# Kernel tuning notes

Hardware: AMD Instinct MI355X
Metric: run time of the kernel (lower is better)

The kernel has to match this reference:

```python
import jax, jax.numpy as jnp
import numpy as np

NUM_GROUP = 512
GROUP_SIZE = 32


def setup_inputs() -> dict:
    key = jax.random.key(0)
    xyz = jax.random.normal(key, (16, 16384, 3), dtype=jnp.float32)
    return {"xyz": xyz}


def reference(xyz):
    B, N, _ = xyz.shape
    # misc.arange-style deterministic center sampling: evenly strided indices
    sel = jnp.arange(NUM_GROUP) * (N // NUM_GROUP)          # [G]
    center = xyz[:, sel, :]                                  # [B, G, 3]

    # squared pairwise distance: ||c||^2 + ||x||^2 - 2 c.x  -> [B, G, N]
    sqr = (-2.0 * jnp.einsum("bgc,bnc->bgn", center, xyz)
           + jnp.sum(center ** 2, axis=-1)[:, :, None]
           + jnp.sum(xyz ** 2, axis=-1)[:, None, :])

    # kNN: smallest K distances -> top_k on negated distances
    _, idx = jax.lax.top_k(-sqr, GROUP_SIZE)                 # [B, G, K]

    # gather neighborhoods per batch: xyz[b, idx[b,g,k], :]
    neighborhood = jax.vmap(lambda pts, i: pts[i])(xyz, idx)  # [B, G, K, 3]
    neighborhood = neighborhood - center[:, :, None, :]

    ids = jnp.broadcast_to(sel[None, :], (B, NUM_GROUP))     # [B, G]
    return neighborhood, center, ids
```

## Files before the change

### kernel.cpp

```cpp
#include <hip/hip_runtime.h>
#include <stdint.h>


#define TB     512
#define GB     8
#define PPT    32
#define NWAVE  (TB / 64)
#define CAP    224

typedef __attribute__((ext_vector_type(2))) float f32x2;

__global__ __launch_bounds__(TB) void group_knn_kernel(
    const float* __restrict__ xyz,
    float* __restrict__ out_nb,
    float* __restrict__ out_ctr,
    float* __restrict__ out_ids)
{
    const int NPTS = 16384;
    const int GSZ  = 32;

    const int blk = blockIdx.x;
    const int b   = blk >> 6;
    const int g0  = (blk & 63) * GB;
    const int t   = threadIdx.x;
    const int lane = t & 63;
    const int w    = t >> 6;

    const float* base = xyz + (size_t)b * NPTS * 3;

    f32x2 C0[GB / 2], C1[GB / 2], C2[GB / 2];
#pragma unroll
    for (int p = 0; p < GB / 2; ++p) {
        const int ncA = (g0 + 2 * p) * 32;
        const int ncB = (g0 + 2 * p + 1) * 32;
        C0[p] = (f32x2){ -2.0f * base[ncA * 3 + 0], -2.0f * base[ncB * 3 + 0] };
        C1[p] = (f32x2){ -2.0f * base[ncA * 3 + 1], -2.0f * base[ncB * 3 + 1] };
        C2[p] = (f32x2){ -2.0f * base[ncA * 3 + 2], -2.0f * base[ncB * 3 + 2] };
    }

    __shared__ unsigned long long s_cand[GB][CAP];
    __shared__ float s_t[GB][NWAVE];
    __shared__ int s_cnt[GB];
    __shared__ unsigned s_win[GB][GSZ];

    f32x2 m2[GB / 2];
#pragma unroll
    for (int p = 0; p < GB / 2; ++p)
        m2[p] = (f32x2){ __builtin_inff(), __builtin_inff() };

    for (int i = 0; i < PPT; i += 4) {
        float px[4][3];
#pragma unroll
        for (int u = 0; u < 4; ++u) {
            const int n = (i + u) * TB + t;
            const float* p = base + (size_t)n * 3;
            px[u][0] = p[0]; px[u][1] = p[1]; px[u][2] = p[2];
        }
#pragma unroll
        for (int u = 0; u < 4; ++u) {
            const float x0 = px[u][0], x1 = px[u][1], x2 = px[u][2];
            const float xs = __builtin_fmaf(x2, x2, __builtin_fmaf(x1, x1, x0 * x0));
            const f32x2 X0 = (f32x2){ x0, x0 };
            const f32x2 X1 = (f32x2){ x1, x1 };
            const f32x2 X2 = (f32x2){ x2, x2 };
            const f32x2 XS = (f32x2){ xs, xs };
#pragma unroll
            for (int p = 0; p < GB / 2; ++p) {
                const f32x2 s = C0[p] * X0 + (C1[p] * X1 + (C2[p] * X2 + XS));
                m2[p] = __builtin_elementwise_min(m2[p], s);
            }
        }
    }

#pragma unroll
    for (int q = 0; q < GB; ++q) {
        float v = (q & 1) ? m2[q >> 1].y : m2[q >> 1].x;
#pragma unroll
        for (int k = 2; k <= 64; k <<= 1) {
#pragma unroll
            for (int j = k >> 1; j > 0; j >>= 1) {
                const float o = __shfl_xor(v, j, 64);
                const bool up = ((lane & k) == 0);
                const bool takeMin = (((lane & j) == 0) == up);
                const float mn = fminf(v, o);
                const float mx = fmaxf(v, o);
                v = takeMin ? mn : mx;
            }
        }
        if (lane == 3) s_t[q][w] = v;
    }
    if (t < GB) s_cnt[t] = 0;
    __syncthreads();

    f32x2 T2[GB / 2];
#pragma unroll
    for (int p = 0; p < GB / 2; ++p) {
        float Ta = s_t[2 * p][0], Tb = s_t[2 * p + 1][0];
#pragma unroll
        for (int ww = 1; ww < NWAVE; ++ww) {
            Ta = fmaxf(Ta, s_t[2 * p][ww]);
            Tb = fmaxf(Tb, s_t[2 * p + 1][ww]);
        }
        T2[p] = (f32x2){ Ta, Tb };
    }

    for (int i = 0; i < PPT; i += 4) {
        float px[4][3];
#pragma unroll
        for (int u = 0; u < 4; ++u) {
            const int n = (i + u) * TB + t;
            const float* p = base + (size_t)n * 3;
            px[u][0] = p[0]; px[u][1] = p[1]; px[u][2] = p[2];
        }
#pragma unroll
        for (int u = 0; u < 4; ++u) {
            const int n = (i + u) * TB + t;
            const float x0 = px[u][0], x1 = px[u][1], x2 = px[u][2];
            const float xs = __builtin_fmaf(x2, x2, __builtin_fmaf(x1, x1, x0 * x0));
            const f32x2 X0 = (f32x2){ x0, x0 };
            const f32x2 X1 = (f32x2){ x1, x1 };
            const f32x2 X2 = (f32x2){ x2, x2 };
            const f32x2 XS = (f32x2){ xs, xs };
#pragma unroll
            for (int p = 0; p < GB / 2; ++p) {
                const f32x2 s = C0[p] * X0 + (C1[p] * X1 + (C2[p] * X2 + XS));
                if (s.x <= T2[p].x) {
                    unsigned uu = __float_as_uint(s.x);
                    uu ^= (unsigned)(((int)uu) >> 31) | 0x80000000u;
                    const int pos = atomicAdd(&s_cnt[2 * p], 1);
                    if (pos < CAP)
                        s_cand[2 * p][pos] = ((unsigned long long)uu << 32) | (unsigned)n;
                }
                if (s.y <= T2[p].y) {
                    unsigned uu = __float_as_uint(s.y);
                    uu ^= (unsigned)(((int)uu) >> 31) | 0x80000000u;
                    const int pos = atomicAdd(&s_cnt[2 * p + 1], 1);
                    if (pos < CAP)
                        s_cand[2 * p + 1][pos] = ((unsigned long long)uu << 32) | (unsigned)n;
                }
            }
        }
    }
    __syncthreads();

    {
        const int q = w;
        const int cnt = s_cnt[q];
        const float Tq = (q & 1) ? T2[q >> 1].y : T2[q >> 1].x;
        const float a0 = (q & 1) ? C0[q >> 1].y : C0[q >> 1].x;
        const float a1 = (q & 1) ? C1[q >> 1].y : C1[q >> 1].x;
        const float a2 = (q & 1) ? C2[q >> 1].y : C2[q >> 1].x;
        (void)Tq;
        if (cnt <= CAP) {
            for (int j = lane; j < cnt; j += 64) {
                const unsigned long long c = s_cand[q][j];
                int r = 0;
                for (int i = 0; i < cnt; ++i) r += (s_cand[q][i] < c) ? 1 : 0;
                if (r < GSZ) s_win[q][r] = (unsigned)c & 0xFFFFu;
            }
        } else {
            unsigned long long last = 0ull;
            for (int k = 0; k < GSZ; ++k) {
                unsigned long long best = ~0ull;
                for (int n = lane; n < NPTS; n += 64) {
                    const float x0 = base[n * 3 + 0];
                    const float x1 = base[n * 3 + 1];
                    const float x2 = base[n * 3 + 2];
                    const float xs = __builtin_fmaf(x2, x2,
                                     __builtin_fmaf(x1, x1, x0 * x0));
                    const float s = __builtin_fmaf(a0, x0,
                                    __builtin_fmaf(a1, x1,
                                    __builtin_fmaf(a2, x2, xs)));
                    unsigned uu = __float_as_uint(s);
                    uu ^= (unsigned)(((int)uu) >> 31) | 0x80000000u;
                    const unsigned long long kk =
                        ((unsigned long long)uu << 32) | (unsigned)n;
                    if (kk > last && kk < best) best = kk;
                }
#pragma unroll
                for (int mm = 32; mm >= 1; mm >>= 1) {
                    const unsigned long long o = __shfl_xor(best, mm, 64);
                    best = (o < best) ? o : best;
                }
                last = best;
                if (lane == 0) s_win[q][k] = (unsigned)best & 0xFFFFu;
            }
        }
    }
    __syncthreads();

    const int gbase = b * 512 + g0;
    if (t < GB * GSZ) {
        const int q  = t >> 5;
        const int tt = t & 31;
        const int nc = (g0 + q) * 32;
        const float cc0 = base[nc * 3 + 0];
        const float cc1 = base[nc * 3 + 1];
        const float cc2 = base[nc * 3 + 2];
        const unsigned n = s_win[q][tt];
        const float x0 = base[n * 3 + 0];
        const float x1 = base[n * 3 + 1];
        const float x2 = base[n * 3 + 2];
        const size_t ob = (((size_t)(gbase + q)) * GSZ + tt) * 3;
        out_nb[ob + 0] = x0 - cc0;
        out_nb[ob + 1] = x1 - cc1;
        out_nb[ob + 2] = x2 - cc2;
    } else if (t < GB * GSZ + GB * 3) {
        const int u = t - GB * GSZ;
        const int q = u / 3, c = u % 3;
        out_ctr[(size_t)(gbase + q) * 3 + c] = base[((g0 + q) * 32) * 3 + c];
    } else if (t < GB * GSZ + GB * 3 + GB) {
        const int q = t - (GB * GSZ + GB * 3);
        out_ids[gbase + q] = (float)((g0 + q) * 32);
    }
}

extern "C" void kernel_launch(void* const* d_in, const int* in_sizes, int n_in,
                              void* d_out, int out_size, void* d_ws, size_t ws_size,
                              hipStream_t stream) {
    const float* xyz = (const float*)d_in[0];
    float* out = (float*)d_out;
    float* out_nb  = out;
    float* out_ctr = out + 786432;
    float* out_ids = out + 786432 + 24576;
    hipLaunchKernelGGL(group_knn_kernel, dim3(16 * 512 / GB), dim3(TB), 0, stream,
                       xyz, out_nb, out_ctr, out_ids);
}
```

Measured before the change: 73.04 us.

## Halve block size and groups per block, add double-buffered point loads

Blocks shrink from 512 to 256 threads and handle 4 centers instead of 8, so 2048 blocks are launched and each thread scans 64 points. Both distance passes now use ping-pong register buffers so the next four points load while the current four are computed, aiming to hide global load latency. The per-wave threshold now takes the 8th-smallest value of each wave's 64 lanes instead of the 4th, so fewer candidates pass the filter with 4 waves. This also doubles the total point-scan work across blocks, since each center pair now rereads the whole cloud in more blocks. The fallback selection gets a small correctness fix for the first iteration.

After: 68.75 us. -5.9%, faster.

```diff
diff --git a/kernel.cpp b/kernel.cpp
--- a/kernel.cpp
+++ b/kernel.cpp
@@ -2,13 +2,77 @@
 #include <stdint.h>
 
 
-#define TB     512
-#define GB     8
-#define PPT    32
+#define TB     256
+#define GB     4
+#define PPT    64
 #define NWAVE  (TB / 64)
 #define CAP    224
 
 typedef __attribute__((ext_vector_type(2))) float f32x2;
+
+#define LOADP(dst, i)                                                    \
+    {                                                                    \
+        _Pragma("unroll")                                                \
+        for (int u = 0; u < 4; ++u) {                                    \
+            const int n = ((i) + u) * TB + t;                            \
+            const float* p = base + (size_t)n * 3;                       \
+            dst[u][0] = p[0]; dst[u][1] = p[1]; dst[u][2] = p[2];        \
+        }                                                                \
+    }
+
+#define COMPA(src)                                                       \
+    {                                                                    \
+        _Pragma("unroll")                                                \
+        for (int u = 0; u < 4; ++u) {                                    \
+            const float x0 = src[u][0], x1 = src[u][1], x2 = src[u][2];  \
+            const float xs = __builtin_fmaf(x2, x2,                      \
+                             __builtin_fmaf(x1, x1, x0 * x0));           \
+            const f32x2 X0 = (f32x2){ x0, x0 };                          \
+            const f32x2 X1 = (f32x2){ x1, x1 };                          \
+            const f32x2 X2 = (f32x2){ x2, x2 };                          \
+            const f32x2 XS = (f32x2){ xs, xs };                          \
+            _Pragma("unroll")                                            \
+            for (int p = 0; p < 2; ++p) {                                \
+                const f32x2 s = C0[p] * X0 + (C1[p] * X1 + (C2[p] * X2 + XS)); \
+                m2[p] = __builtin_elementwise_min(m2[p], s);             \
+            }                                                            \
+        }                                                                \
+    }
+
+#define COMPB(src, i)                                                    \
+    {                                                                    \
+        _Pragma("unroll")                                                \
+        for (int u = 0; u < 4; ++u) {                                    \
+            const int n = ((i) + u) * TB + t;                            \
+            const float x0 = src[u][0], x1 = src[u][1], x2 = src[u][2];  \
+            const float xs = __builtin_fmaf(x2, x2,                      \
+                             __builtin_fmaf(x1, x1, x0 * x0));           \
+            const f32x2 X0 = (f32x2){ x0, x0 };                          \
+            const f32x2 X1 = (f32x2){ x1, x1 };                          \
+            const f32x2 X2 = (f32x2){ x2, x2 };                          \
+            const f32x2 XS = (f32x2){ xs, xs };                          \
+            _Pragma("unroll")                                            \
+            for (int p = 0; p < 2; ++p) {                                \
+                const f32x2 s = C0[p] * X0 + (C1[p] * X1 + (C2[p] * X2 + XS)); \
+                if (s.x <= T2[p].x) {                                    \
+                    unsigned uu = __float_as_uint(s.x);                  \
+                    uu ^= (unsigned)(((int)uu) >> 31) | 0x80000000u;     \
+                    const int pos = atomicAdd(&s_cnt[2 * p], 1);         \
+                    if (pos < CAP)                                       \
+                        s_cand[2 * p][pos] =                             \
+                            ((unsigned long long)uu << 32) | (unsigned)n;\
+                }                                                        \
+                if (s.y <= T2[p].y) {                                    \
+                    unsigned uu = __float_as_uint(s.y);                  \
+                    uu ^= (unsigned)(((int)uu) >> 31) | 0x80000000u;     \
+                    const int pos = atomicAdd(&s_cnt[2 * p + 1], 1);     \
+                    if (pos < CAP)                                       \
+                        s_cand[2 * p + 1][pos] =                         \
+                            ((unsigned long long)uu << 32) | (unsigned)n;\
+                }                                                        \
+            }                                                            \
+        }                                                                \
+    }
 
 __global__ __launch_bounds__(TB) void group_knn_kernel(
     const float* __restrict__ xyz,
@@ -20,17 +84,17 @@
     const int GSZ  = 32;
 
     const int blk = blockIdx.x;
-    const int b   = blk >> 6;
-    const int g0  = (blk & 63) * GB;
+    const int b   = blk >> 7;
+    const int g0  = (blk & 127) * GB;
     const int t   = threadIdx.x;
     const int lane = t & 63;
     const int w    = t >> 6;
 
     const float* base = xyz + (size_t)b * NPTS * 3;
 
-    f32x2 C0[GB / 2], C1[GB / 2], C2[GB / 2];
-#pragma unroll
-    for (int p = 0; p < GB / 2; ++p) {
+    f32x2 C0[2], C1[2], C2[2];
+#pragma unroll
+    for (int p = 0; p < 2; ++p) {
         const int ncA = (g0 + 2 * p) * 32;
         const int ncB = (g0 + 2 * p + 1) * 32;
         C0[p] = (f32x2){ -2.0f * base[ncA * 3 + 0], -2.0f * base[ncB * 3 + 0] };
@@ -43,32 +107,19 @@
     __shared__ int s_cnt[GB];
     __shared__ unsigned s_win[GB][GSZ];
 
-    f32x2 m2[GB / 2];
-#pragma unroll
-    for (int p = 0; p < GB / 2; ++p)
+    f32x2 m2[2];
+#pragma unroll
+    for (int p = 0; p < 2; ++p)
         m2[p] = (f32x2){ __builtin_inff(), __builtin_inff() };
 
-    for (int i = 0; i < PPT; i += 4) {
-        float px[4][3];
-#pragma unroll
-        for (int u = 0; u < 4; ++u) {
-            const int n = (i + u) * TB + t;
-            const float* p = base + (size_t)n * 3;
-            px[u][0] = p[0]; px[u][1] = p[1]; px[u][2] = p[2];
-        }
-#pragma unroll
-        for (int u = 0; u < 4; ++u) {
-            const float x0 = px[u][0], x1 = px[u][1], x2 = px[u][2];
-            const float xs = __builtin_fmaf(x2, x2, __builtin_fmaf(x1, x1, x0 * x0));
-            const f32x2 X0 = (f32x2){ x0, x0 };
-            const f32x2 X1 = (f32x2){ x1, x1 };
-            const f32x2 X2 = (f32x2){ x2, x2 };
-            const f32x2 XS = (f32x2){ xs, xs };
-#pragma unroll
-            for (int p = 0; p < GB / 2; ++p) {
-                const f32x2 s = C0[p] * X0 + (C1[p] * X1 + (C2[p] * X2 + XS));
-                m2[p] = __builtin_elementwise_min(m2[p], s);
-            }
+    {
+        float pa[4][3], pb[4][3];
+        LOADP(pa, 0);
+        for (int i = 0; i < PPT; i += 8) {
+            LOADP(pb, i + 4);
+            COMPA(pa);
+            if (i + 8 < PPT) LOADP(pa, i + 8);
+            COMPA(pb);
         }
     }
 
@@ -87,14 +138,14 @@
                 v = takeMin ? mn : mx;
             }
         }
-        if (lane == 3) s_t[q][w] = v;
+        if (lane == 7) s_t[q][w] = v;
     }
     if (t < GB) s_cnt[t] = 0;
     __syncthreads();
 
-    f32x2 T2[GB / 2];
-#pragma unroll
-    for (int p = 0; p < GB / 2; ++p) {
+    f32x2 T2[2];
+#pragma unroll
+    for (int p = 0; p < 2; ++p) {
         float Ta = s_t[2 * p][0], Tb = s_t[2 * p + 1][0];
 #pragma unroll
         for (int ww = 1; ww < NWAVE; ++ww) {
@@ -104,41 +155,14 @@
         T2[p] = (f32x2){ Ta, Tb };
     }
 
-    for (int i = 0; i < PPT; i += 4) {
-        float px[4][3];
-#pragma unroll
-        for (int u = 0; u < 4; ++u) {
-            const int n = (i + u) * TB + t;
-            const float* p = base + (size_t)n * 3;
-            px[u][0] = p[0]; px[u][1] = p[1]; px[u][2] = p[2];
-        }
-#pragma unroll
-        for (int u = 0; u < 4; ++u) {
-            const int n = (i + u) * TB + t;
-            const float x0 = px[u][0], x1 = px[u][1], x2 = px[u][2];
-            const float xs = __builtin_fmaf(x2, x2, __builtin_fmaf(x1, x1, x0 * x0));
-            const f32x2 X0 = (f32x2){ x0, x0 };
-            const f32x2 X1 = (f32x2){ x1, x1 };
-            const f32x2 X2 = (f32x2){ x2, x2 };
-            const f32x2 XS = (f32x2){ xs, xs };
-#pragma unroll
-            for (int p = 0; p < GB / 2; ++p) {
-                const f32x2 s = C0[p] * X0 + (C1[p] * X1 + (C2[p] * X2 + XS));
-                if (s.x <= T2[p].x) {
-                    unsigned uu = __float_as_uint(s.x);
-                    uu ^= (unsigned)(((int)uu) >> 31) | 0x80000000u;
-                    const int pos = atomicAdd(&s_cnt[2 * p], 1);
-                    if (pos < CAP)
-                        s_cand[2 * p][pos] = ((unsigned long long)uu << 32) | (unsigned)n;
-                }
-                if (s.y <= T2[p].y) {
-                    unsigned uu = __float_as_uint(s.y);
-                    uu ^= (unsigned)(((int)uu) >> 31) | 0x80000000u;
-                    const int pos = atomicAdd(&s_cnt[2 * p + 1], 1);
-                    if (pos < CAP)
-                        s_cand[2 * p + 1][pos] = ((unsigned long long)uu << 32) | (unsigned)n;
-                }
-            }
+    {
+        float pa[4][3], pb[4][3];
+        LOADP(pa, 0);
+        for (int i = 0; i < PPT; i += 8) {
+            LOADP(pb, i + 4);
+            COMPB(pa, i);
+            if (i + 8 < PPT) LOADP(pa, i + 8);
+            COMPB(pb, i + 4);
         }
     }
     __syncthreads();
@@ -146,11 +170,9 @@
     {
         const int q = w;
         const int cnt = s_cnt[q];
-        const float Tq = (q & 1) ? T2[q >> 1].y : T2[q >> 1].x;
         const float a0 = (q & 1) ? C0[q >> 1].y : C0[q >> 1].x;
         const float a1 = (q & 1) ? C1[q >> 1].y : C1[q >> 1].x;
         const float a2 = (q & 1) ? C2[q >> 1].y : C2[q >> 1].x;
-        (void)Tq;
         if (cnt <= CAP) {
             for (int j = lane; j < cnt; j += 64) {
                 const unsigned long long c = s_cand[q][j];
@@ -175,7 +197,7 @@
                     uu ^= (unsigned)(((int)uu) >> 31) | 0x80000000u;
                     const unsigned long long kk =
                         ((unsigned long long)uu << 32) | (unsigned)n;
-                    if (kk > last && kk < best) best = kk;
+                    if ((k == 0 || kk > last) && kk < best) best = kk;
                 }
 #pragma unroll
                 for (int mm = 32; mm >= 1; mm >>= 1) {
@@ -223,6 +245,6 @@
     float* out_nb  = out;
     float* out_ctr = out + 786432;
     float* out_ids = out + 786432 + 24576;
-    hipLaunchKernelGGL(group_knn_kernel, dim3(16 * 512 / GB), dim3(TB), 0, stream,
+    hipLaunchKernelGGL(group_knn_kernel, dim3(2048), dim3(TB), 0, stream,
                        xyz, out_nb, out_ctr, out_ids);
 }
```

## Shrink blocks to two groups and 128 threads with more points per thread

Applied to the files above, without the earlier changes.

Each block now handles 2 centers with 128 threads instead of 8 centers with 512 threads, and each thread scans 128 points. The launch grows to 4096 blocks. The threshold now uses the 16th-smallest per-wave minimum, and the candidate capacity rises to 320. The aim is more blocks and lower per-block register and shared-memory pressure. The cost is that every point load is shared by only 2 centers instead of 8, so global/L2 traffic per unit of distance work roughly quadruples. The looser threshold also yields more candidates for the quadratic rank step. It also fixes the fallback selection so the first pick accepts key zero.

Result: slower. 77.07 us (+5.5%).

```diff
diff --git a/kernel.cpp b/kernel.cpp
--- a/kernel.cpp
+++ b/kernel.cpp
@@ -2,11 +2,11 @@
 #include <stdint.h>
 
 
-#define TB     512
-#define GB     8
-#define PPT    32
+#define TB     128
+#define GB     2
+#define PPT    128
 #define NWAVE  (TB / 64)
-#define CAP    224
+#define CAP    320
 
 typedef __attribute__((ext_vector_type(2))) float f32x2;
 
@@ -20,22 +20,21 @@
     const int GSZ  = 32;
 
     const int blk = blockIdx.x;
-    const int b   = blk >> 6;
-    const int g0  = (blk & 63) * GB;
+    const int b   = blk >> 8;
+    const int g0  = (blk & 255) * GB;
     const int t   = threadIdx.x;
     const int lane = t & 63;
     const int w    = t >> 6;
 
     const float* base = xyz + (size_t)b * NPTS * 3;
 
-    f32x2 C0[GB / 2], C1[GB / 2], C2[GB / 2];
-#pragma unroll
-    for (int p = 0; p < GB / 2; ++p) {
-        const int ncA = (g0 + 2 * p) * 32;
-        const int ncB = (g0 + 2 * p + 1) * 32;
-        C0[p] = (f32x2){ -2.0f * base[ncA * 3 + 0], -2.0f * base[ncB * 3 + 0] };
-        C1[p] = (f32x2){ -2.0f * base[ncA * 3 + 1], -2.0f * base[ncB * 3 + 1] };
-        C2[p] = (f32x2){ -2.0f * base[ncA * 3 + 2], -2.0f * base[ncB * 3 + 2] };
+    f32x2 C0, C1, C2;
+    {
+        const int ncA = g0 * 32;
+        const int ncB = (g0 + 1) * 32;
+        C0 = (f32x2){ -2.0f * base[ncA * 3 + 0], -2.0f * base[ncB * 3 + 0] };
+        C1 = (f32x2){ -2.0f * base[ncA * 3 + 1], -2.0f * base[ncB * 3 + 1] };
+        C2 = (f32x2){ -2.0f * base[ncA * 3 + 2], -2.0f * base[ncB * 3 + 2] };
     }
 
     __shared__ unsigned long long s_cand[GB][CAP];
@@ -43,10 +42,7 @@
     __shared__ int s_cnt[GB];
     __shared__ unsigned s_win[GB][GSZ];
 
-    f32x2 m2[GB / 2];
-#pragma unroll
-    for (int p = 0; p < GB / 2; ++p)
-        m2[p] = (f32x2){ __builtin_inff(), __builtin_inff() };
+    f32x2 m2 = (f32x2){ __builtin_inff(), __builtin_inff() };
 
     for (int i = 0; i < PPT; i += 4) {
         float px[4][3];
@@ -64,17 +60,14 @@
             const f32x2 X1 = (f32x2){ x1, x1 };
             const f32x2 X2 = (f32x2){ x2, x2 };
             const f32x2 XS = (f32x2){ xs, xs };
-#pragma unroll
-            for (int p = 0; p < GB / 2; ++p) {
-                const f32x2 s = C0[p] * X0 + (C1[p] * X1 + (C2[p] * X2 + XS));
-                m2[p] = __builtin_elementwise_min(m2[p], s);
-            }
+            const f32x2 s = C0 * X0 + (C1 * X1 + (C2 * X2 + XS));
+            m2 = __builtin_elementwise_min(m2, s);
         }
     }
 
 #pragma unroll
     for (int q = 0; q < GB; ++q) {
-        float v = (q & 1) ? m2[q >> 1].y : m2[q >> 1].x;
+        float v = (q & 1) ? m2.y : m2.x;
 #pragma unroll
         for (int k = 2; k <= 64; k <<= 1) {
 #pragma unroll
@@ -87,21 +80,20 @@
                 v = takeMin ? mn : mx;
             }
         }
-        if (lane == 3) s_t[q][w] = v;
+        if (lane == 15) s_t[q][w] = v;
     }
     if (t < GB) s_cnt[t] = 0;
     __syncthreads();
 
-    f32x2 T2[GB / 2];
-#pragma unroll
-    for (int p = 0; p < GB / 2; ++p) {
-        float Ta = s_t[2 * p][0], Tb = s_t[2 * p + 1][0];
+    f32x2 T2;
+    {
+        float Ta = s_t[0][0], Tb = s_t[1][0];
 #pragma unroll
         for (int ww = 1; ww < NWAVE; ++ww) {
-            Ta = fmaxf(Ta, s_t[2 * p][ww]);
-            Tb = fmaxf(Tb, s_t[2 * p + 1][ww]);
-        }
-        T2[p] = (f32x2){ Ta, Tb };
+            Ta = fmaxf(Ta, s_t[0][ww]);
+            Tb = fmaxf(Tb, s_t[1][ww]);
+        }
+        T2 = (f32x2){ Ta, Tb };
     }
 
     for (int i = 0; i < PPT; i += 4) {
@@ -121,23 +113,20 @@
             const f32x2 X1 = (f32x2){ x1, x1 };
             const f32x2 X2 = (f32x2){ x2, x2 };
             const f32x2 XS = (f32x2){ xs, xs };
-#pragma unroll
-            for (int p = 0; p < GB / 2; ++p) {
-                const f32x2 s = C0[p] * X0 + (C1[p] * X1 + (C2[p] * X2 + XS));
-                if (s.x <= T2[p].x) {
-                    unsigned uu = __float_as_uint(s.x);
-                    uu ^= (unsigned)(((int)uu) >> 31) | 0x80000000u;
-                    const int pos = atomicAdd(&s_cnt[2 * p], 1);
-                    if (pos < CAP)
-                        s_cand[2 * p][pos] = ((unsigned long long)uu << 32) | (unsigned)n;
-                }
-                if (s.y <= T2[p].y) {
-                    unsigned uu = __float_as_uint(s.y);
-                    uu ^= (unsigned)(((int)uu) >> 31) | 0x80000000u;
-                    const int pos = atomicAdd(&s_cnt[2 * p + 1], 1);
-                    if (pos < CAP)
-                        s_cand[2 * p + 1][pos] = ((unsigned long long)uu << 32) | (unsigned)n;
-                }
+            const f32x2 s = C0 * X0 + (C1 * X1 + (C2 * X2 + XS));
+            if (s.x <= T2.x) {
+                unsigned uu = __float_as_uint(s.x);
+                uu ^= (unsigned)(((int)uu) >> 31) | 0x80000000u;
+                const int pos = atomicAdd(&s_cnt[0], 1);
+                if (pos < CAP)
+                    s_cand[0][pos] = ((unsigned long long)uu << 32) | (unsigned)n;
+            }
+            if (s.y <= T2.y) {
+                unsigned uu = __float_as_uint(s.y);
+                uu ^= (unsigned)(((int)uu) >> 31) | 0x80000000u;
+                const int pos = atomicAdd(&s_cnt[1], 1);
+                if (pos < CAP)
+                    s_cand[1][pos] = ((unsigned long long)uu << 32) | (unsigned)n;
             }
         }
     }
@@ -146,11 +135,9 @@
     {
         const int q = w;
         const int cnt = s_cnt[q];
-        const float Tq = (q & 1) ? T2[q >> 1].y : T2[q >> 1].x;
-        const float a0 = (q & 1) ? C0[q >> 1].y : C0[q >> 1].x;
-        const float a1 = (q & 1) ? C1[q >> 1].y : C1[q >> 1].x;
-        const float a2 = (q & 1) ? C2[q >> 1].y : C2[q >> 1].x;
-        (void)Tq;
+        const float a0 = q ? C0.y : C0.x;
+        const float a1 = q ? C1.y : C1.x;
+        const float a2 = q ? C2.y : C2.x;
         if (cnt <= CAP) {
             for (int j = lane; j < cnt; j += 64) {
                 const unsigned long long c = s_cand[q][j];
@@ -175,7 +162,7 @@
                     uu ^= (unsigned)(((int)uu) >> 31) | 0x80000000u;
                     const unsigned long long kk =
                         ((unsigned long long)uu << 32) | (unsigned)n;
-                    if (kk > last && kk < best) best = kk;
+                    if ((k == 0 || kk > last) && kk < best) best = kk;
                 }
 #pragma unroll
                 for (int mm = 32; mm >= 1; mm >>= 1) {
@@ -223,6 +210,6 @@
     float* out_nb  = out;
     float* out_ctr = out + 786432;
     float* out_ids = out + 786432 + 24576;
-    hipLaunchKernelGGL(group_knn_kernel, dim3(16 * 512 / GB), dim3(TB), 0, stream,
+    hipLaunchKernelGGL(group_knn_kernel, dim3(4096), dim3(TB), 0, stream,
                        xyz, out_nb, out_ctr, out_ids);
 }
```
